# Kernel tuning notes

Measured on AMD Instinct MI355X. Metric: run time of the kernel, lower is better.

Reference implementation:

```python
import jax, jax.numpy as jnp
import numpy as np

B, C, T = 32, 1024, 1024
BETA = 0.95      # snn.Leaky(beta=0.95)
THR = 1.0        # snntorch Leaky default threshold
SIGMA_INIT = 10.5  # mean of sigma_range (1, 20)


def _gaussian_matrix(sigma, channels):
    # row i is the Gaussian pdf over x=0..C-1 centered at mean=i (vectorized
    # form of the source's per-row Python loop; identical values).
    x = jnp.arange(channels, dtype=jnp.float32)
    u = (x[None, :] - x[:, None]) / sigma  # [C, C]
    coef = 1.0 / (sigma * jnp.sqrt(jnp.asarray(2.0 * jnp.pi, dtype=jnp.float32)))
    return coef * jnp.exp(-0.5 * u * u)


def _spike(u):
    # heaviside(u) forward; ATan surrogate gradient (snntorch default, alpha=2)
    soft = jnp.arctan(jnp.pi * u) / jnp.pi
    hard = (u > 0).astype(u.dtype)
    return soft + jax.lax.stop_gradient(hard - soft)


def setup_inputs() -> dict:
    key = jax.random.key(0)
    inp = jax.random.normal(key, (B, C, T), dtype=jnp.float32)
    sigma = jnp.ones((1,), dtype=jnp.float32) * SIGMA_INIT
    return {"inp": inp, "sigma": sigma}


def reference(inp, sigma):
    # inp: [B, C, T], sigma: [1]
    s = sigma[0]
    w = _gaussian_matrix(s, inp.shape[1])  # computed once: identical at every t
    # I[b,i,t] = x[b,i,t] - sum_j w[i,j] * x[b,j,t]
    I = inp - jnp.einsum('ij,bjt->bit', w, inp)
    I_tbc = jnp.moveaxis(I, 2, 0)  # [T, B, C]

    def step(mem, It):
        # snntorch Leaky (reset_mechanism='subtract'):
        # reset fires on incoming mem, then decay+integrate, then spike.
        reset = _spike(mem - THR)
        mem = BETA * mem + It - reset * THR
        spk = _spike(mem - THR)
        return mem, spk

    mem0 = jnp.zeros(I_tbc.shape[1:], dtype=inp.dtype)  # [B, C]
    _, spks = jax.lax.scan(step, mem0, I_tbc)  # spks: [T, B, C]
    return jnp.moveaxis(spks, 0, 2)  # [B, C, T]
```

## Files before the change

### kernel.cpp

```cpp
#include <hip/hip_runtime.h>
#include <math.h>

#define B_   32
#define C_   1024
#define T_   1024
#define RT   92
#define CT   64
#define TT   64
#define KC   8
#define NTY  (CT/KC)
#define ROWS (CT + 2*RT)
#define NJJ  (2*RT + KC)
#define WN   (2*(RT + KC - 1) + 1)
#define WOFF (RT + KC - 1)
#define NF4  (ROWS * (TT/4))
#define NSTG 8

__device__ __forceinline__ float tap_value(float s, int d) {
    float u    = __fdiv_rn((float)d, s);
    float t1   = __fmul_rn(-0.5f, u);
    float t2   = __fmul_rn(t1, u);
    float e    = (float)exp((double)t2);
    float den  = __fmul_rn(s, sqrtf(6.2831854820251465f));
    float coef = __fdiv_rn(1.0f, den);
    return __fmul_rn(coef, e);
}

__global__ void init_w_kernel(const float* __restrict__ sigma, float* __restrict__ gw) {
    int i = threadIdx.x;
    if (i < WN) {
        int d = i - WOFF;
        gw[i] = (d >= -RT && d <= RT) ? tap_value(sigma[0], d) : 0.0f;
    }
}

template <bool GW>
__global__ __launch_bounds__(512, 4) void snn_v5(
    const float* __restrict__ x, const float* __restrict__ sigma,
    const float* __restrict__ gw, float* __restrict__ out)
{
    __shared__ __align__(16) float xs[ROWS * TT];
    __shared__ float Is[CT * 65];
    __shared__ float wl[GW ? 1 : WN];

    const int tx   = threadIdx.x;
    const int ty   = threadIdx.y;
    const int flat = ty * 64 + tx;
    const int b    = blockIdx.y;
    const int c0   = blockIdx.x * CT;

    if (!GW) {
        if (flat < WN) {
            int d = flat - WOFF;
            wl[flat] = (d >= -RT && d <= RT) ? tap_value(sigma[0], d) : 0.0f;
        }
    }

    const float* xb = x   + (size_t)b * ((size_t)C_ * T_);
    float*       ob = out + (size_t)b * ((size_t)C_ * T_);

    float4 stg[NSTG];

#define STAGE_LOAD(T0)                                                         \
    _Pragma("unroll")                                                          \
    for (int i = 0; i < NSTG; ++i) {                                           \
        int e = flat + i * 512;                                                \
        float4 v = make_float4(0.f, 0.f, 0.f, 0.f);                            \
        if (e < NF4) {                                                         \
            int r = e >> 4, c4v = e & 15;                                      \
            int c = c0 - RT + r;                                               \
            if (c >= 0 && c < C_)                                              \
                v = *(const float4*)(xb + (size_t)c * T_ + (T0) + c4v * 4);    \
        }                                                                      \
        stg[i] = v;                                                            \
    }

#define STAGE_WRITE()                                                          \
    _Pragma("unroll")                                                          \
    for (int i = 0; i < NSTG; ++i) {                                           \
        int e = flat + i * 512;                                                \
        if (e < NF4) *(float4*)(xs + (size_t)e * 4) = stg[i];                  \
    }

    STAGE_LOAD(0);

    float mem = 0.0f;
    const int rb = ty * KC;

    for (int kk = 0; kk < T_ / TT; ++kk) {
        const int t0 = kk * TT;

        STAGE_WRITE();
        __syncthreads();

        if (kk < T_ / TT - 1) { STAGE_LOAD(t0 + TT); }

        float acc[KC];
#pragma unroll
        for (int k = 0; k < KC; ++k) acc[k] = 0.0f;

#pragma unroll 8
        for (int jj = 0; jj < NJJ; ++jj) {
            float xv = xs[(rb + jj) * TT + tx];
#pragma unroll
            for (int k = 0; k < KC; ++k) {
                float wv = GW ? gw[jj + (KC - 1) - k] : wl[jj + (KC - 1) - k];
                acc[k] = fmaf(wv, xv, acc[k]);
            }
        }
#pragma unroll
        for (int k = 0; k < KC; ++k) {
            float xo = xs[(rb + RT + k) * TT + tx];
            Is[(rb + k) * 65 + tx] = __fsub_rn(xo, acc[k]);
        }
        __syncthreads();

        if (flat < 64) {
            float m = mem;
            float* orow = ob + (size_t)(c0 + flat) * T_ + t0;
#pragma unroll
            for (int tq = 0; tq < TT / 4; ++tq) {
                float4 s;
#pragma unroll
                for (int q = 0; q < 4; ++q) {
                    float Ivv = Is[flat * 65 + tq * 4 + q];
                    float r   = (m > 1.0f) ? 1.0f : 0.0f;
                    m = __fsub_rn(__fadd_rn(__fmul_rn(0.95f, m), Ivv), r);
                    float sp  = (m > 1.0f) ? 1.0f : 0.0f;
                    if (q == 0) s.x = sp; else if (q == 1) s.y = sp;
                    else if (q == 2) s.z = sp; else s.w = sp;
                }
                *(float4*)(orow + tq * 4) = s;
            }
            mem = m;
        }
        __syncthreads();
    }
#undef STAGE_LOAD
#undef STAGE_WRITE
}

extern "C" void kernel_launch(void* const* d_in, const int* in_sizes, int n_in,
                              void* d_out, int out_size, void* d_ws, size_t ws_size,
                              hipStream_t stream) {
    const float* x     = (const float*)d_in[0];
    const float* sigma = (const float*)d_in[1];
    float* out = (float*)d_out;

    dim3 grid(C_ / CT, B_);
    dim3 block(64, NTY);

    if (ws_size >= WN * sizeof(float)) {
        float* gw = (float*)d_ws;
        init_w_kernel<<<1, 256, 0, stream>>>(sigma, gw);
        snn_v5<true><<<grid, block, 0, stream>>>(x, sigma, gw, out);
    } else {
        snn_v5<false><<<grid, block, 0, stream>>>(x, sigma, nullptr, out);
    }
}
```

Before: 181.9 us.

## Transpose shared x tile for float4 channel reads and per-warp LIF scan

Stores the staged input tile transposed (time-major, padded stride 252) so each thread reads its channel window as float4 vectors in the banded convolution. The spiking scan is now done per warp-row group on its own strip of currents, by 8 threads per ty group instead of 64 threads of one group. This removes the barrier between the convolution and the scan. It is meant to cut LDS instruction count and the serialization of the scan. The transposed scalar stores into shared memory may cause bank conflicts, and the fallback path now recomputes taps inline.

```diff
diff --git a/kernel.cpp b/kernel.cpp
--- a/kernel.cpp
+++ b/kernel.cpp
@@ -1,20 +1,20 @@
 #include <hip/hip_runtime.h>
 #include <math.h>
 
-#define B_   32
-#define C_   1024
-#define T_   1024
-#define RT   92
-#define CT   64
-#define TT   64
-#define KC   8
-#define NTY  (CT/KC)
-#define ROWS (CT + 2*RT)
-#define NJJ  (2*RT + KC)
-#define WN   (2*(RT + KC - 1) + 1)
-#define WOFF (RT + KC - 1)
-#define NF4  (ROWS * (TT/4))
-#define NSTG 8
+#define B_     32
+#define C_     1024
+#define T_     1024
+#define RT     92
+#define CT     64
+#define TT     64
+#define KC     8
+#define NTY    8
+#define NJQ    48
+#define WN     (2*(RT + KC - 1) + 1)
+#define WOFF   (RT + KC - 1)
+#define NCOLS  (CT + 2*RT)
+#define XSTR   252
+#define ISTR   68
 
 __device__ __forceinline__ float tap_value(float s, int d) {
     float u    = __fdiv_rn((float)d, s);
@@ -35,57 +35,65 @@
 }
 
 template <bool GW>
-__global__ __launch_bounds__(512, 4) void snn_v5(
+__global__ __launch_bounds__(512, 4) void snn_v6(
     const float* __restrict__ x, const float* __restrict__ sigma,
     const float* __restrict__ gw, float* __restrict__ out)
 {
-    __shared__ __align__(16) float xs[ROWS * TT];
-    __shared__ float Is[CT * 65];
-    __shared__ float wl[GW ? 1 : WN];
+    __shared__ __align__(16) float xsT[TT * XSTR];
+    __shared__ __align__(16) float IsS[NTY * KC * ISTR];
 
     const int tx   = threadIdx.x;
     const int ty   = threadIdx.y;
     const int flat = ty * 64 + tx;
     const int b    = blockIdx.y;
     const int c0   = blockIdx.x * CT;
-
-    if (!GW) {
-        if (flat < WN) {
-            int d = flat - WOFF;
-            wl[flat] = (d >= -RT && d <= RT) ? tap_value(sigma[0], d) : 0.0f;
-        }
-    }
+    const int rb   = ty * KC;
 
     const float* xb = x   + (size_t)b * ((size_t)C_ * T_);
     float*       ob = out + (size_t)b * ((size_t)C_ * T_);
 
-    float4 stg[NSTG];
+    float sv = 0.0f;
+    if (!GW) sv = sigma[0];
 
-#define STAGE_LOAD(T0)                                                         \
-    _Pragma("unroll")                                                          \
-    for (int i = 0; i < NSTG; ++i) {                                           \
-        int e = flat + i * 512;                                                \
-        float4 v = make_float4(0.f, 0.f, 0.f, 0.f);                            \
-        if (e < NF4) {                                                         \
-            int r = e >> 4, c4v = e & 15;                                      \
-            int c = c0 - RT + r;                                               \
-            if (c >= 0 && c < C_)                                              \
-                v = *(const float4*)(xb + (size_t)c * T_ + (T0) + c4v * 4);    \
-        }                                                                      \
-        stg[i] = v;                                                            \
+    float4 stg[2][4];
+    const int rB  = (flat >> 2);
+    const int c4B = (flat & 3);
+
+#define STAGE_LOAD(T0)                                                          \
+    _Pragma("unroll")                                                           \
+    for (int i1 = 0; i1 < 2; ++i1) {                                            \
+        _Pragma("unroll")                                                       \
+        for (int i2 = 0; i2 < 4; ++i2) {                                        \
+            int r  = rB + 128 * i1;                                             \
+            int c4 = c4B + 4 * i2;                                              \
+            int c  = c0 - RT + r;                                               \
+            float4 v = make_float4(0.f, 0.f, 0.f, 0.f);                         \
+            if (r < NCOLS && c >= 0 && c < C_)                                  \
+                v = *(const float4*)(xb + (size_t)c * T_ + (T0) + c4 * 4);      \
+            stg[i1][i2] = v;                                                    \
+        }                                                                       \
     }
 
-#define STAGE_WRITE()                                                          \
-    _Pragma("unroll")                                                          \
-    for (int i = 0; i < NSTG; ++i) {                                           \
-        int e = flat + i * 512;                                                \
-        if (e < NF4) *(float4*)(xs + (size_t)e * 4) = stg[i];                  \
+#define STAGE_WRITE()                                                           \
+    _Pragma("unroll")                                                           \
+    for (int i1 = 0; i1 < 2; ++i1) {                                            \
+        _Pragma("unroll")                                                       \
+        for (int i2 = 0; i2 < 4; ++i2) {                                        \
+            int r  = rB + 128 * i1;                                             \
+            int c4 = c4B + 4 * i2;                                              \
+            if (r < NCOLS) {                                                    \
+                xsT[(4 * c4 + 0) * XSTR + r] = stg[i1][i2].x;                   \
+                xsT[(4 * c4 + 1) * XSTR + r] = stg[i1][i2].y;                   \
+                xsT[(4 * c4 + 2) * XSTR + r] = stg[i1][i2].z;                   \
+                xsT[(4 * c4 + 3) * XSTR + r] = stg[i1][i2].w;                   \
+            }                                                                   \
+        }                                                                       \
     }
 
     STAGE_LOAD(0);
 
     float mem = 0.0f;
-    const int rb = ty * KC;
+    float* strip = IsS + ty * (KC * ISTR);
 
     for (int kk = 0; kk < T_ / TT; ++kk) {
         const int t0 = kk * TT;
@@ -99,38 +107,54 @@
 #pragma unroll
         for (int k = 0; k < KC; ++k) acc[k] = 0.0f;
 
-#pragma unroll 8
-        for (int jj = 0; jj < NJJ; ++jj) {
-            float xv = xs[(rb + jj) * TT + tx];
+        const float* xrow = &xsT[tx * XSTR + rb];
+#pragma unroll 4
+        for (int jq = 0; jq < NJQ; ++jq) {
+            float4 xv = *(const float4*)(xrow + 4 * jq);
 #pragma unroll
-            for (int k = 0; k < KC; ++k) {
-                float wv = GW ? gw[jj + (KC - 1) - k] : wl[jj + (KC - 1) - k];
-                acc[k] = fmaf(wv, xv, acc[k]);
+            for (int qq = 0; qq < 4; ++qq) {
+                float xs1 = (qq == 0) ? xv.x : (qq == 1) ? xv.y : (qq == 2) ? xv.z : xv.w;
+#pragma unroll
+                for (int k = 0; k < KC; ++k) {
+                    float wv;
+                    if (GW) {
+                        wv = gw[4 * jq + qq + 7 - k];
+                    } else {
+                        int d = 4 * jq + qq + 7 - k - WOFF;
+                        wv = (d >= -RT && d <= RT) ? tap_value(sv, d) : 0.0f;
+                    }
+                    acc[k] = fmaf(wv, xs1, acc[k]);
+                }
             }
         }
+
+        float4 xoA = *(const float4*)(xrow + RT);
+        float4 xoB = *(const float4*)(xrow + RT + 4);
+        {
+            float xo[KC] = {xoA.x, xoA.y, xoA.z, xoA.w, xoB.x, xoB.y, xoB.z, xoB.w};
 #pragma unroll
-        for (int k = 0; k < KC; ++k) {
-            float xo = xs[(rb + RT + k) * TT + tx];
-            Is[(rb + k) * 65 + tx] = __fsub_rn(xo, acc[k]);
+            for (int k = 0; k < KC; ++k)
+                strip[k * ISTR + tx] = __fsub_rn(xo[k], acc[k]);
         }
-        __syncthreads();
 
-        if (flat < 64) {
+        if (tx < KC) {
             float m = mem;
-            float* orow = ob + (size_t)(c0 + flat) * T_ + t0;
-#pragma unroll
-            for (int tq = 0; tq < TT / 4; ++tq) {
+            const float* srow = strip + tx * ISTR;
+            float* orow = ob + (size_t)(c0 + rb + tx) * T_ + t0;
+#pragma unroll 4
+            for (int q = 0; q < TT / 4; ++q) {
+                float4 Iq = *(const float4*)(srow + 4 * q);
                 float4 s;
 #pragma unroll
-                for (int q = 0; q < 4; ++q) {
-                    float Ivv = Is[flat * 65 + tq * 4 + q];
+                for (int qq = 0; qq < 4; ++qq) {
+                    float Ivv = (qq == 0) ? Iq.x : (qq == 1) ? Iq.y : (qq == 2) ? Iq.z : Iq.w;
                     float r   = (m > 1.0f) ? 1.0f : 0.0f;
                     m = __fsub_rn(__fadd_rn(__fmul_rn(0.95f, m), Ivv), r);
                     float sp  = (m > 1.0f) ? 1.0f : 0.0f;
-                    if (q == 0) s.x = sp; else if (q == 1) s.y = sp;
-                    else if (q == 2) s.z = sp; else s.w = sp;
+                    if (qq == 0) s.x = sp; else if (qq == 1) s.y = sp;
+                    else if (qq == 2) s.z = sp; else s.w = sp;
                 }
-                *(float4*)(orow + tq * 4) = s;
+                *(float4*)(orow + 4 * q) = s;
             }
             mem = m;
         }
@@ -153,8 +177,8 @@
     if (ws_size >= WN * sizeof(float)) {
         float* gw = (float*)d_ws;
         init_w_kernel<<<1, 256, 0, stream>>>(sigma, gw);
-        snn_v5<true><<<grid, block, 0, stream>>>(x, sigma, gw, out);
+        snn_v6<true><<<grid, block, 0, stream>>>(x, sigma, gw, out);
     } else {
-        snn_v5<false><<<grid, block, 0, stream>>>(x, sigma, nullptr, out);
+        snn_v6<false><<<grid, block, 0, stream>>>(x, sigma, nullptr, out);
     }
 }
```

After: 186.0 us. 2.3% more time.
